# Performance work log

Measured on AMD Instinct MI355X. Metric: run time of the kernel, lower is better.

## Reference

```python
import jax, jax.numpy as jnp
import numpy as np

N = 50000      # active voxels
CIN = 128
COUT = 128
K = 3          # kernel_size
GRID = 128     # voxel grid side


def _build_neighbor_map(rng):
    """Replicates hash_module.mapping_cuda: for each voxel n and kernel offset k,
    nbr[k, n] = row index of voxel at coords[n] + offset_k, or -1 if not active."""
    lin = rng.choice(GRID ** 3, size=N, replace=False)
    coords = np.stack(np.unravel_index(lin, (GRID, GRID, GRID)), axis=1).astype(np.int32)
    lut = np.full(GRID ** 3, -1, dtype=np.int32)
    lut[lin] = np.arange(N, dtype=np.int32)
    offsets = np.array([(dx, dy, dz)
                        for dx in (-1, 0, 1)
                        for dy in (-1, 0, 1)
                        for dz in (-1, 0, 1)], dtype=np.int32)
    nbr = np.full((K ** 3, N), -1, dtype=np.int32)
    for k, off in enumerate(offsets):
        nc = coords + off[None, :]
        valid = ((nc >= 0) & (nc < GRID)).all(axis=1)
        l = (nc[:, 0].astype(np.int64) * GRID + nc[:, 1]) * GRID + nc[:, 2]
        nbr[k, valid] = lut[l[valid]]
    return nbr


def setup_inputs() -> dict:
    rng = np.random.default_rng(0)
    nbr = _build_neighbor_map(rng)
    key = jax.random.key(0)
    k1, k2 = jax.random.split(key)
    feats = jax.random.normal(k1, (N, CIN), dtype=jnp.float32)
    stdv = 1.0 / np.sqrt(COUT * K ** 3)  # matches reset_parameters
    kernel = jax.random.uniform(k2, (K ** 3, CIN, COUT), dtype=jnp.float32,
                                minval=-stdv, maxval=stdv)
    return {"feats": feats, "kernel": kernel, "nbr_idx": jnp.asarray(nbr)}


def reference(feats, kernel, nbr_idx):
    # Submanifold sparse conv: out[n] = sum_k feats[nbr_idx[k, n]] @ kernel[k]
    # (zero contribution where no active neighbor). Scan over the 27 offsets
    # to avoid materializing the [27, N, Cin] gathered tensor.
    out0 = jnp.zeros((feats.shape[0], kernel.shape[-1]), dtype=feats.dtype)

    def body(acc, ko):
        idx, w = ko                              # idx: [N], w: [Cin, Cout]
        mask = idx >= 0
        g = feats[jnp.where(mask, idx, 0)]       # safe gather [N, Cin]
        g = jnp.where(mask[:, None], g, 0.0)
        return acc + g @ w, None

    out, _ = jax.lax.scan(body, out0, (nbr_idx, kernel))
    return out
```

## Files before the change

kernel.cpp:

```cpp
#include <hip/hip_runtime.h>
#include <stddef.h>

#define CIN  128
#define COUT 128
#define KK   27
#define CAP  256
#define CMAX 255
#define EMAX 96

typedef short bf16x8 __attribute__((ext_vector_type(8)));
typedef float f32x4  __attribute__((ext_vector_type(4)));

__device__ __forceinline__ short f2bf(float f) {
    unsigned u = __float_as_uint(f);
    unsigned r = (u + 0x7fffu + ((u >> 16) & 1u)) >> 16;
    return (short)r;
}
__device__ __forceinline__ float bf2f(short s) {
    unsigned u = ((unsigned)(unsigned short)s) << 16;
    return __uint_as_float(u);
}

#define PACK_UNITS (KK * 4 * 8 * 64)
#define PACKB ((PACK_UNITS + 255) / 256)

__global__ __launch_bounds__(256) void pack_W(
    const float* __restrict__ W, short* __restrict__ Wp)
{
    int fl = blockIdx.x * 256 + threadIdx.x;
    if (fl >= PACK_UNITS) return;
    int lane = fl & 63, nf = (fl >> 6) & 7, ks = (fl >> 9) & 3, k = fl >> 11;
    int col  = nf * 16 + (lane & 15);
    int krow = ks * 32 + (lane >> 4) * 8;
    bf16x8 v;
    #pragma unroll
    for (int j = 0; j < 8; ++j)
        v[j] = f2bf(W[((size_t)k * CIN + krow + j) * COUT + col]);
    *reinterpret_cast<bf16x8*>(Wp + (size_t)fl * 8) = v;
}

__global__ __launch_bounds__(256) void fused_gemm(
    const short* __restrict__ Wp, const int* __restrict__ nbr,
    const float* __restrict__ feats, int N, int nsb, int nbk,
    unsigned char* __restrict__ pos, short* __restrict__ partial,
    float* __restrict__ out)
{
    __shared__ short Asub[64 * 128];
    const int t = threadIdx.x;
    const int wave = t >> 6, lane = t & 63;
    const int lrow = lane & 15, lhi = lane >> 4;

    if ((int)blockIdx.x >= nbk) {
        const int tile0 = ((int)blockIdx.x - nbk) * 64;
        const short* Wp13 = Wp + (size_t)13 * 16384;

        #pragma unroll
        for (int j = 0; j < 4; ++j) {
            int slot = t + 256 * j;
            int row = slot >> 4, cg = slot & 15;
            int r = tile0 + row;
            bf16x8 v = {0,0,0,0,0,0,0,0};
            if (r < N) {
                const float* fr = feats + (size_t)r * CIN + cg * 8;
                float4 x = *reinterpret_cast<const float4*>(fr);
                float4 y = *reinterpret_cast<const float4*>(fr + 4);
                v = bf16x8{ f2bf(x.x), f2bf(x.y), f2bf(x.z), f2bf(x.w),
                            f2bf(y.x), f2bf(y.y), f2bf(y.z), f2bf(y.w) };
            }
            int sw = cg ^ (row & 7);
            *reinterpret_cast<bf16x8*>(&Asub[row * 128 + sw * 8]) = v;
        }

        bf16x8 bfr[2][4];
        #pragma unroll
        for (int nf = 0; nf < 2; ++nf)
            #pragma unroll
            for (int ks = 0; ks < 4; ++ks)
                bfr[nf][ks] = *reinterpret_cast<const bf16x8*>(
                    Wp13 + ((size_t)(ks * 8 + wave * 2 + nf) * 64 + lane) * 8);

        __syncthreads();

        f32x4 zero = {0.f, 0.f, 0.f, 0.f};
        f32x4 acc[4][2];
        #pragma unroll
        for (int mf = 0; mf < 4; ++mf) { acc[mf][0] = zero; acc[mf][1] = zero; }

        #pragma unroll
        for (int ks = 0; ks < 4; ++ks)
            #pragma unroll
            for (int mf = 0; mf < 4; ++mf) {
                int row = mf * 16 + lrow;
                int sw = (ks * 4 + lhi) ^ (lrow & 7);
                bf16x8 a = *reinterpret_cast<const bf16x8*>(&Asub[row * 128 + sw * 8]);
                acc[mf][0] = __builtin_amdgcn_mfma_f32_16x16x32_bf16(a, bfr[0][ks], acc[mf][0], 0, 0, 0);
                acc[mf][1] = __builtin_amdgcn_mfma_f32_16x16x32_bf16(a, bfr[1][ks], acc[mf][1], 0, 0, 0);
            }

        #pragma unroll
        for (int mf = 0; mf < 4; ++mf)
            #pragma unroll
            for (int nf = 0; nf < 2; ++nf)
                #pragma unroll
                for (int j = 0; j < 4; ++j) {
                    int r = tile0 + mf * 16 + lhi * 4 + j;
                    if (r < N)
                        out[(size_t)r * COUT + wave * 32 + nf * 16 + lrow] = acc[mf][nf][j];
                }
        return;
    }

    const int b = blockIdx.x;
    const int k = b / nsb, sb = b - k * nsb;
    if (k == 13) return;

    __shared__ int2 plds[CAP];
    __shared__ int cw[32];
    __shared__ int sbase, scap;

    const int* nk = nbr + (size_t)k * N;
    unsigned char* posk = pos + (size_t)k * N;

    int nsrc[8];
    #pragma unroll
    for (int c = 0; c < 8; ++c) {
        int n = sb * 2048 + c * 256 + t;
        nsrc[c] = (n < N) ? nk[n] : -1;
    }
    int pfx[8];
    const unsigned long long lmask = (1ull << lane) - 1ull;
    #pragma unroll
    for (int c = 0; c < 8; ++c) {
        unsigned long long m = __ballot(nsrc[c] >= 0);
        pfx[c] = __popcll(m & lmask);
        if (lane == 0) cw[c * 4 + wave] = __popcll(m);
    }
    __syncthreads();
    if (t == 0) {
        int a = 0;
        #pragma unroll
        for (int i = 0; i < 32; ++i) { int v = cw[i]; cw[i] = a; a += v; }
        sbase = a;
        scap = (a < CMAX) ? a : CMAX;
    }
    __syncthreads();
    #pragma unroll
    for (int c = 0; c < 8; ++c) {
        int n = sb * 2048 + c * 256 + t;
        bool valid = (nsrc[c] >= 0);
        int off = cw[c * 4 + wave] + pfx[c];
        bool kept = valid && (off < CMAX);
        if (kept) plds[off] = make_int2(n, nsrc[c]);
        if (n < N) posk[n] = kept ? (unsigned char)off : (unsigned char)255;
    }
    const int cnt0 = scap;
    if (cnt0 == 0) return;

    bf16x8 bfr[2][4];
    #pragma unroll
    for (int nf = 0; nf < 2; ++nf)
        #pragma unroll
        for (int ks = 0; ks < 4; ++ks)
            bfr[nf][ks] = *reinterpret_cast<const bf16x8*>(
                Wp + ((size_t)((k * 4 + ks) * 8 + wave * 2 + nf) * 64 + lane) * 8);

    for (int t0 = 0; t0 < cnt0; t0 += 64) {
        __syncthreads();
        #pragma unroll
        for (int j = 0; j < 4; ++j) {
            int slot = t + 256 * j;
            int row = slot >> 4, cg = slot & 15;
            int srow = t0 + row;
            bf16x8 v = {0,0,0,0,0,0,0,0};
            if (srow < cnt0) {
                int src = plds[srow].y;
                const float* fr = feats + (size_t)src * CIN + cg * 8;
                float4 x = *reinterpret_cast<const float4*>(fr);
                float4 y = *reinterpret_cast<const float4*>(fr + 4);
                v = bf16x8{ f2bf(x.x), f2bf(x.y), f2bf(x.z), f2bf(x.w),
                            f2bf(y.x), f2bf(y.y), f2bf(y.z), f2bf(y.w) };
            }
            int sw = cg ^ (row & 7);
            *reinterpret_cast<bf16x8*>(&Asub[row * 128 + sw * 8]) = v;
        }
        __syncthreads();

        f32x4 zero = {0.f, 0.f, 0.f, 0.f};
        f32x4 acc[4][2];
        #pragma unroll
        for (int mf = 0; mf < 4; ++mf) { acc[mf][0] = zero; acc[mf][1] = zero; }

        #pragma unroll
        for (int ks = 0; ks < 4; ++ks)
            #pragma unroll
            for (int mf = 0; mf < 4; ++mf) {
                int row = mf * 16 + lrow;
                int sw = (ks * 4 + lhi) ^ (lrow & 7);
                bf16x8 a = *reinterpret_cast<const bf16x8*>(&Asub[row * 128 + sw * 8]);
                acc[mf][0] = __builtin_amdgcn_mfma_f32_16x16x32_bf16(a, bfr[0][ks], acc[mf][0], 0, 0, 0);
                acc[mf][1] = __builtin_amdgcn_mfma_f32_16x16x32_bf16(a, bfr[1][ks], acc[mf][1], 0, 0, 0);
            }

        #pragma unroll
        for (int mf = 0; mf < 4; ++mf)
            #pragma unroll
            for (int j = 0; j < 4; ++j) {
                int slot = t0 + mf * 16 + lhi * 4 + j;
                if (slot >= cnt0) continue;
                short* dst = partial + ((size_t)b * CAP + slot) * COUT + wave * 32 + lrow;
                dst[0]  = f2bf(acc[mf][0][j]);
                dst[16] = f2bf(acc[mf][1][j]);
            }
    }
}

__global__ __launch_bounds__(256) void scatter_add(
    const unsigned char* __restrict__ pos, const short* __restrict__ partial,
    float* __restrict__ out, int N, int nsb)
{
    __shared__ short Pbuf[EMAX][136];
    __shared__ short erowL[EMAX];
    __shared__ int   eidxL[EMAX];
    __shared__ int   kcnt[KK], koff[KK];
    __shared__ int   eTotS;

    const int tile0 = blockIdx.x * 64;
    const int sbk = tile0 >> 11;
    const int t = threadIdx.x;
    const int wave = t >> 6, lane = t & 63;

    int pv[7];
    #pragma unroll
    for (int rd = 0; rd < 7; ++rd) {
        int k = rd * 4 + wave;
        pv[rd] = 255;
        if (k < KK && k != 13 && tile0 + lane < N)
            pv[rd] = (int)pos[(size_t)k * N + tile0 + lane];
    }
    int mypfx[7];
    const unsigned long long lmask = (1ull << lane) - 1ull;
    #pragma unroll
    for (int rd = 0; rd < 7; ++rd) {
        int k = rd * 4 + wave;
        unsigned long long m = __ballot(pv[rd] != 255);
        mypfx[rd] = __popcll(m & lmask);
        if (k < KK && lane == 0) kcnt[k] = __popcll(m);
    }
    __syncthreads();
    if (t == 0) {
        int a = 0;
        for (int k = 0; k < KK; ++k) { koff[k] = a; a += kcnt[k]; }
        eTotS = (a < EMAX) ? a : EMAX;
    }
    __syncthreads();
    #pragma unroll
    for (int rd = 0; rd < 7; ++rd) {
        int k = rd * 4 + wave;
        if (k < KK && pv[rd] != 255) {
            int s = koff[k] + mypfx[rd];
            if (s < EMAX) {
                erowL[s] = (short)lane;
                eidxL[s] = ((k * nsb + sbk) * CAP) + pv[rd];
            }
        }
    }
    __syncthreads();
    const int eTot = eTotS;
    if (eTot == 0) return;

    for (int e = t >> 4; e < eTot; e += 16) {
        int sub = t & 15;
        *reinterpret_cast<bf16x8*>(&Pbuf[e][sub * 8]) =
            *reinterpret_cast<const bf16x8*>(partial + (size_t)eidxL[e] * COUT + sub * 8);
    }
    __syncthreads();

    const int r = t >> 2, q = t & 3;
    float acc[32];
    #pragma unroll
    for (int i = 0; i < 32; ++i) acc[i] = 0.f;
    bool any = false;

    #pragma unroll 1
    for (int e = 0; e < eTot; ++e) {
        if ((int)erowL[e] != r) continue;
        any = true;
        #pragma unroll
        for (int v8 = 0; v8 < 4; ++v8) {
            bf16x8 p = *reinterpret_cast<const bf16x8*>(&Pbuf[e][q * 32 + v8 * 8]);
            #pragma unroll
            for (int j = 0; j < 8; ++j) acc[v8 * 8 + j] += bf2f(p[j]);
        }
    }

    if (any && tile0 + r < N) {
        float* dst = out + (size_t)(tile0 + r) * COUT + q * 32;
        #pragma unroll
        for (int v4 = 0; v4 < 8; ++v4) {
            float4 o = *reinterpret_cast<float4*>(dst + v4 * 4);
            o.x += acc[v4 * 4 + 0]; o.y += acc[v4 * 4 + 1];
            o.z += acc[v4 * 4 + 2]; o.w += acc[v4 * 4 + 3];
            *reinterpret_cast<float4*>(dst + v4 * 4) = o;
        }
    }
}

__global__ __launch_bounds__(128) void naive_spconv(
    const float* __restrict__ feats, const float* __restrict__ Wbase,
    const int* __restrict__ nbr, float* __restrict__ out, int N)
{
    int n  = blockIdx.x;
    int co = threadIdx.x;
    __shared__ float frow[CIN];
    float acc = 0.f;
    for (int k = 0; k < KK; ++k) {
        int src = nbr[(size_t)k * N + n];
        if (src < 0) continue;
        __syncthreads();
        frow[co] = feats[(size_t)src * CIN + co];
        __syncthreads();
        const float* Wk = Wbase + (size_t)k * CIN * COUT;
        #pragma unroll 8
        for (int ci = 0; ci < CIN; ++ci)
            acc = fmaf(frow[ci], Wk[ci * COUT + co], acc);
    }
    out[(size_t)n * COUT + co] = acc;
}

extern "C" void kernel_launch(void* const* d_in, const int* in_sizes, int n_in,
                              void* d_out, int out_size, void* d_ws, size_t ws_size,
                              hipStream_t stream) {
    const float* feats = (const float*)d_in[0];
    const float* Wb    = (const float*)d_in[1];
    const int*   nbr   = (const int*)d_in[2];
    float* out = (float*)d_out;
    const int N = in_sizes[0] / CIN;
    const int nsb = (N + 2047) >> 11;
    const int nbk = KK * nsb;
    const int ctiles = (N + 63) / 64;

    size_t off_wp   = 0;
    size_t off_pos  = ((size_t)PACK_UNITS * 8 * 2 + 255) & ~(size_t)255;
    size_t off_part = (off_pos + (size_t)KK * N + 255) & ~(size_t)255;
    size_t need = off_part + (size_t)nbk * CAP * COUT * 2;

    if (ws_size >= need) {
        short*         wp   = (short*)((char*)d_ws + off_wp);
        unsigned char* pos  = (unsigned char*)((char*)d_ws + off_pos);
        short*         part = (short*)((char*)d_ws + off_part);

        pack_W<<<PACKB, 256, 0, stream>>>(Wb, wp);
        fused_gemm<<<nbk + ctiles, 256, 0, stream>>>(wp, nbr, feats, N, nsb, nbk,
                                                     pos, part, out);
        scatter_add<<<ctiles, 256, 0, stream>>>(pos, part, out, N, nsb);
    } else {
        naive_spconv<<<N, 128, 0, stream>>>(feats, Wb, nbr, out, N);
    }
}
```

Before: 39.89 us.

## Drop weight-pack kernel, load fp32 weights directly, halve gather superblock size

```diff
diff --git a/kernel.cpp b/kernel.cpp
--- a/kernel.cpp
+++ b/kernel.cpp
@@ -4,8 +4,9 @@
 #define CIN  128
 #define COUT 128
 #define KK   27
-#define CAP  256
-#define CMAX 255
+#define SBS  1024
+#define CAP  128
+#define CMAX 127
 #define EMAX 96
 
 typedef short bf16x8 __attribute__((ext_vector_type(8)));
@@ -21,26 +22,25 @@
     return __uint_as_float(u);
 }
 
-#define PACK_UNITS (KK * 4 * 8 * 64)
-#define PACKB ((PACK_UNITS + 255) / 256)
-
-__global__ __launch_bounds__(256) void pack_W(
-    const float* __restrict__ W, short* __restrict__ Wp)
+__device__ __forceinline__ void load_bfr(
+    const float* __restrict__ W, int k, int wave, int lrow, int lhi,
+    bf16x8 bfr[2][4])
 {
-    int fl = blockIdx.x * 256 + threadIdx.x;
-    if (fl >= PACK_UNITS) return;
-    int lane = fl & 63, nf = (fl >> 6) & 7, ks = (fl >> 9) & 3, k = fl >> 11;
-    int col  = nf * 16 + (lane & 15);
-    int krow = ks * 32 + (lane >> 4) * 8;
-    bf16x8 v;
-    #pragma unroll
-    for (int j = 0; j < 8; ++j)
-        v[j] = f2bf(W[((size_t)k * CIN + krow + j) * COUT + col]);
-    *reinterpret_cast<bf16x8*>(Wp + (size_t)fl * 8) = v;
+    #pragma unroll
+    for (int nf = 0; nf < 2; ++nf)
+        #pragma unroll
+        for (int ks = 0; ks < 4; ++ks) {
+            const float* base = W + ((size_t)k * CIN + ks * 32 + lhi * 8) * COUT
+                                  + wave * 32 + nf * 16 + lrow;
+            bf16x8 v;
+            #pragma unroll
+            for (int j = 0; j < 8; ++j) v[j] = f2bf(base[(size_t)j * COUT]);
+            bfr[nf][ks] = v;
+        }
 }
 
 __global__ __launch_bounds__(256) void fused_gemm(
-    const short* __restrict__ Wp, const int* __restrict__ nbr,
+    const float* __restrict__ W, const int* __restrict__ nbr,
     const float* __restrict__ feats, int N, int nsb, int nbk,
     unsigned char* __restrict__ pos, short* __restrict__ partial,
     float* __restrict__ out)
@@ -52,7 +52,6 @@
 
     if ((int)blockIdx.x >= nbk) {
         const int tile0 = ((int)blockIdx.x - nbk) * 64;
-        const short* Wp13 = Wp + (size_t)13 * 16384;
 
         #pragma unroll
         for (int j = 0; j < 4; ++j) {
@@ -72,12 +71,7 @@
         }
 
         bf16x8 bfr[2][4];
-        #pragma unroll
-        for (int nf = 0; nf < 2; ++nf)
-            #pragma unroll
-            for (int ks = 0; ks < 4; ++ks)
-                bfr[nf][ks] = *reinterpret_cast<const bf16x8*>(
-                    Wp13 + ((size_t)(ks * 8 + wave * 2 + nf) * 64 + lane) * 8);
+        load_bfr(W, 13, wave, lrow, lhi, bfr);
 
         __syncthreads();
 
@@ -115,38 +109,41 @@
     if (k == 13) return;
 
     __shared__ int2 plds[CAP];
-    __shared__ int cw[32];
-    __shared__ int sbase, scap;
+    __shared__ int cw[16];
+    __shared__ int scap;
 
     const int* nk = nbr + (size_t)k * N;
     unsigned char* posk = pos + (size_t)k * N;
 
-    int nsrc[8];
-    #pragma unroll
-    for (int c = 0; c < 8; ++c) {
-        int n = sb * 2048 + c * 256 + t;
+    int nsrc[4];
+    #pragma unroll
+    for (int c = 0; c < 4; ++c) {
+        int n = sb * SBS + c * 256 + t;
         nsrc[c] = (n < N) ? nk[n] : -1;
     }
-    int pfx[8];
+    int pfx[4];
     const unsigned long long lmask = (1ull << lane) - 1ull;
     #pragma unroll
-    for (int c = 0; c < 8; ++c) {
+    for (int c = 0; c < 4; ++c) {
         unsigned long long m = __ballot(nsrc[c] >= 0);
         pfx[c] = __popcll(m & lmask);
         if (lane == 0) cw[c * 4 + wave] = __popcll(m);
     }
+
+    bf16x8 bfr[2][4];
+    load_bfr(W, k, wave, lrow, lhi, bfr);
+
     __syncthreads();
     if (t == 0) {
         int a = 0;
         #pragma unroll
-        for (int i = 0; i < 32; ++i) { int v = cw[i]; cw[i] = a; a += v; }
-        sbase = a;
+        for (int i = 0; i < 16; ++i) { int v = cw[i]; cw[i] = a; a += v; }
         scap = (a < CMAX) ? a : CMAX;
     }
     __syncthreads();
     #pragma unroll
-    for (int c = 0; c < 8; ++c) {
-        int n = sb * 2048 + c * 256 + t;
+    for (int c = 0; c < 4; ++c) {
+        int n = sb * SBS + c * 256 + t;
         bool valid = (nsrc[c] >= 0);
         int off = cw[c * 4 + wave] + pfx[c];
         bool kept = valid && (off < CMAX);
@@ -155,14 +152,6 @@
     }
     const int cnt0 = scap;
     if (cnt0 == 0) return;
-
-    bf16x8 bfr[2][4];
-    #pragma unroll
-    for (int nf = 0; nf < 2; ++nf)
-        #pragma unroll
-        for (int ks = 0; ks < 4; ++ks)
-            bfr[nf][ks] = *reinterpret_cast<const bf16x8*>(
-                Wp + ((size_t)((k * 4 + ks) * 8 + wave * 2 + nf) * 64 + lane) * 8);
 
     for (int t0 = 0; t0 < cnt0; t0 += 64) {
         __syncthreads();
@@ -225,7 +214,7 @@
     __shared__ int   eTotS;
 
     const int tile0 = blockIdx.x * 64;
-    const int sbk = tile0 >> 11;
+    const int sbk = tile0 / SBS;
     const int t = threadIdx.x;
     const int wave = t >> 6, lane = t & 63;
 
@@ -335,22 +324,19 @@
     const int*   nbr   = (const int*)d_in[2];
     float* out = (float*)d_out;
     const int N = in_sizes[0] / CIN;
-    const int nsb = (N + 2047) >> 11;
+    const int nsb = (N + SBS - 1) / SBS;
     const int nbk = KK * nsb;
     const int ctiles = (N + 63) / 64;
 
-    size_t off_wp   = 0;
-    size_t off_pos  = ((size_t)PACK_UNITS * 8 * 2 + 255) & ~(size_t)255;
-    size_t off_part = (off_pos + (size_t)KK * N + 255) & ~(size_t)255;
+    size_t off_pos  = 0;
+    size_t off_part = (((size_t)KK * N) + 255) & ~(size_t)255;
     size_t need = off_part + (size_t)nbk * CAP * COUT * 2;
 
     if (ws_size >= need) {
-        short*         wp   = (short*)((char*)d_ws + off_wp);
         unsigned char* pos  = (unsigned char*)((char*)d_ws + off_pos);
         short*         part = (short*)((char*)d_ws + off_part);
 
-        pack_W<<<PACKB, 256, 0, stream>>>(Wb, wp);
-        fused_gemm<<<nbk + ctiles, 256, 0, stream>>>(wp, nbr, feats, N, nsb, nbk,
+        fused_gemm<<<nbk + ctiles, 256, 0, stream>>>(Wb, nbr, feats, N, nsb, nbk,
                                                      pos, part, out);
         scatter_add<<<ctiles, 256, 0, stream>>>(pos, part, out, N, nsb);
     } else {
```

Measured after the change: 43.67 us. +9.5%, slower.
